# Kernel tuning notes

Hardware: AMD Instinct MI355X
Metric: run time of the kernel (lower is better)

Reference implementation:

```python
import jax, jax.numpy as jnp
import numpy as np

D_MODEL = 1024
NUM_HEADS = 16
HEAD_DIM = D_MODEL // NUM_HEADS
WINDOW = 256
NEG = -1000000000.0


def setup_inputs() -> dict:
    key = jax.random.key(0)
    ks = jax.random.split(key, 9)
    B, N, D = 2, 2048, D_MODEL
    s = 1.0 / np.sqrt(D)
    inp = {
        "x": jax.random.normal(ks[0], (B, N, D), dtype=jnp.float32),
        "Wq": jax.random.normal(ks[1], (D, D), dtype=jnp.float32) * s,
        "bq": jnp.zeros((D,), dtype=jnp.float32),
        "Wk": jax.random.normal(ks[2], (D, D), dtype=jnp.float32) * s,
        "bk": jnp.zeros((D,), dtype=jnp.float32),
        "Wv": jax.random.normal(ks[3], (D, D), dtype=jnp.float32) * s,
        "bv": jnp.zeros((D,), dtype=jnp.float32),
        "Wo": jax.random.normal(ks[4], (D, D), dtype=jnp.float32) * s,
        "bo": jnp.zeros((D,), dtype=jnp.float32),
    }
    return inp


def reference(x, Wq, bq, Wk, bk, Wv, bv, Wo, bo):
    B, N, D = x.shape
    H, hd = NUM_HEADS, HEAD_DIM
    q = (x @ Wq + bq).reshape(B, N, H, hd).transpose(0, 2, 1, 3)  # [B,H,N,hd]
    k = (x @ Wk + bk).reshape(B, N, H, hd).transpose(0, 2, 1, 3)
    v = (x @ Wv + bv).reshape(B, N, H, hd).transpose(0, 2, 1, 3)

    i = jnp.arange(N)[:, None]
    j = jnp.arange(N)[None, :]
    blocked = (j > i) | (j < i - WINDOW)  # causal + local window
    mask = jnp.where(blocked, jnp.float32(NEG), jnp.float32(0.0))  # [N,N]

    logits = jnp.einsum("bhid,bhjd->bhij", q, k) / jnp.sqrt(jnp.float32(hd))
    logits = logits + mask[None, None, :, :]
    attn = jax.nn.softmax(logits, axis=-1)
    out = jnp.einsum("bhij,bhjd->bhid", attn, v)  # [B,H,N,hd]
    out = out.transpose(0, 2, 1, 3).reshape(B, N, D)
    return out @ Wo + bo
```

## Files before the change

kernel.cpp:

```cpp
#include <hip/hip_runtime.h>


typedef unsigned short ushort_t;
typedef __bf16 bf16x8 __attribute__((ext_vector_type(8)));
typedef float f32x4 __attribute__((ext_vector_type(4)));
typedef unsigned short ushort8 __attribute__((ext_vector_type(8)));
typedef unsigned short ushort4v __attribute__((ext_vector_type(4)));

#define LOG2E 1.4426950408889634f

static __device__ __forceinline__ ushort_t f2b(float f) {
    union { float f; unsigned int u; } x;
    x.f = f;
    unsigned int u = x.u;
    unsigned int r = (u + 0x7FFFu + ((u >> 16) & 1u)) >> 16;
    return (ushort_t)r;
}

static __device__ __forceinline__ void store_out(float* p, float v) { *p = v; }
static __device__ __forceinline__ void store_out(ushort_t* p, float v) { *p = f2b(v); }

static __device__ __forceinline__ int sw(int row, int c) {
    return (row * 8 + (c ^ (row & 7))) * 8;
}

static __device__ __forceinline__ void gload_lds16(const ushort_t* g, ushort_t* l) {
    __builtin_amdgcn_global_load_lds(
        (const __attribute__((address_space(1))) void*)g,
        (__attribute__((address_space(3))) void*)l, 16, 0, 0);
}

__global__ __launch_bounds__(256) void prep_kernel(
    const float* __restrict__ x, ushort_t* __restrict__ xbf,
    const float* __restrict__ W0, const float* __restrict__ W1,
    const float* __restrict__ W2, const float* __restrict__ W3,
    ushort_t* __restrict__ T0, ushort_t* __restrict__ T1,
    ushort_t* __restrict__ T2, ushort_t* __restrict__ T3) {
    int tx = threadIdx.x, ty = threadIdx.y;
    if (blockIdx.z == 4) {
        int idx = (blockIdx.y * 32 + blockIdx.x) * 256 + ty * 32 + tx;
        int i = idx * 16;
#pragma unroll
        for (int half = 0; half < 2; half++) {
            f32x4 a = *(const f32x4*)&x[i + half * 8];
            f32x4 b = *(const f32x4*)&x[i + half * 8 + 4];
            ushort8 o;
#pragma unroll
            for (int e = 0; e < 4; e++) o[e] = f2b(a[e]);
#pragma unroll
            for (int e = 0; e < 4; e++) o[4 + e] = f2b(b[e]);
            *(ushort8*)&xbf[i + half * 8] = o;
        }
        return;
    }
    __shared__ ushort_t tile[32][33];
    const float* W;
    ushort_t* T;
    switch (blockIdx.z) {
        case 0: W = W0; T = T0; break;
        case 1: W = W1; T = T1; break;
        case 2: W = W2; T = T2; break;
        default: W = W3; T = T3; break;
    }
    int xx = blockIdx.x * 32 + tx;
    int ybase = blockIdx.y * 32 + ty;
#pragma unroll
    for (int r = 0; r < 4; r++) tile[ty + r * 8][tx] = f2b(W[(ybase + r * 8) * 1024 + xx]);
    __syncthreads();
    int xo = blockIdx.y * 32 + tx;
    int yobase = blockIdx.x * 32 + ty;
#pragma unroll
    for (int r = 0; r < 4; r++) T[(yobase + r * 8) * 1024 + xo] = tile[tx][ty + r * 8];
}

__global__ __launch_bounds__(256) void gemm_qkv_kernel(
    const ushort_t* __restrict__ A,
    const ushort_t* __restrict__ Bt0, const ushort_t* __restrict__ Bt1,
    const ushort_t* __restrict__ Bt2,
    const float* __restrict__ bias0, const float* __restrict__ bias1,
    const float* __restrict__ bias2,
    ushort_t* __restrict__ C0, ushort_t* __restrict__ C1, ushort_t* __restrict__ C2,
    float os0, float os1, float os2) {
    __shared__ ushort_t Al[64 * 64];
    __shared__ ushort_t Bl[128 * 64];

    const int id = blockIdx.x;
    const int xcd = id & 7;
    const int s = id >> 3;
    int m_blk = (xcd >> 1) * 16 + (s & 15);
    int ncol = (xcd & 1) * 12 + (s >> 4);
    int zsel = ncol >> 3;
    ncol &= 7;
    const int m0 = m_blk * 64;
    const int n0 = ncol * 128;

    const ushort_t* Bt;
    const float* bias;
    ushort_t* C;
    float oscale;
    if (zsel == 0) { Bt = Bt0; bias = bias0; C = C0; oscale = os0; }
    else if (zsel == 1) { Bt = Bt1; bias = bias1; C = C1; oscale = os1; }
    else { Bt = Bt2; bias = bias2; C = C2; oscale = os2; }

    const int tid = threadIdx.x;
    const int w = tid >> 6;
    const int l = tid & 63;
    const int wm = (w >> 1) * 32;
    const int wn = (w & 1) * 64;
    const int lrow = l & 15;
    const int lq = l >> 4;

    f32x4 acc[2][4];
#pragma unroll
    for (int mi = 0; mi < 2; mi++)
#pragma unroll
        for (int ni = 0; ni < 4; ni++) acc[mi][ni] = 0.0f;

    const int kt0 = (id * 5) & 15;
    for (int it = 0; it < 16; it++) {
        const int kt = ((kt0 + it) & 15) * 64;
#pragma unroll
        for (int t = 0; t < 2; t++) {
            int idx = t * 256 + tid;
            int row = idx >> 3, cs = idx & 7, c = cs ^ (row & 7);
            gload_lds16(&A[(long)(m0 + row) * 1024 + kt + c * 8], &Al[idx * 8]);
        }
#pragma unroll
        for (int t = 0; t < 4; t++) {
            int idx = t * 256 + tid;
            int row = idx >> 3, cs = idx & 7, c = cs ^ (row & 7);
            gload_lds16(&Bt[(long)(n0 + row) * 1024 + kt + c * 8], &Bl[idx * 8]);
        }
        __syncthreads();
#pragma unroll
        for (int ks = 0; ks < 64; ks += 32) {
            const int cb = (ks >> 3) + lq;
            bf16x8 af[2], bfr[4];
#pragma unroll
            for (int mi = 0; mi < 2; mi++)
                af[mi] = *(const bf16x8*)&Al[sw(wm + mi * 16 + lrow, cb)];
#pragma unroll
            for (int ni = 0; ni < 4; ni++)
                bfr[ni] = *(const bf16x8*)&Bl[sw(wn + ni * 16 + lrow, cb)];
#pragma unroll
            for (int mi = 0; mi < 2; mi++)
#pragma unroll
                for (int ni = 0; ni < 4; ni++)
                    acc[mi][ni] = __builtin_amdgcn_mfma_f32_16x16x32_bf16(
                        af[mi], bfr[ni], acc[mi][ni], 0, 0, 0);
        }
        __syncthreads();
    }

    if (zsel == 2) {
#pragma unroll
        for (int ni = 0; ni < 4; ni++) {
            int n = n0 + wn + ni * 16 + lrow;
            float bv = bias[n];
#pragma unroll
            for (int mi = 0; mi < 2; mi++) {
                int m = m0 + wm + mi * 16 + lq * 4;
                ushort4v o;
#pragma unroll
                for (int r = 0; r < 4; r++) o[r] = f2b((acc[mi][ni][r] + bv) * oscale);
                *(ushort4v*)&C[(long)n * 4096 + m] = o;
            }
        }
    } else {
#pragma unroll
        for (int ni = 0; ni < 4; ni++) {
            int n = n0 + wn + ni * 16 + lrow;
            float bv = bias[n];
#pragma unroll
            for (int mi = 0; mi < 2; mi++) {
#pragma unroll
                for (int r = 0; r < 4; r++) {
                    int m = m0 + wm + mi * 16 + lq * 4 + r;
                    store_out(&C[(long)m * 1024 + n], (acc[mi][ni][r] + bv) * oscale);
                }
            }
        }
    }
}

__global__ __launch_bounds__(256) void gemm_out_kernel(
    const ushort_t* __restrict__ A, const ushort_t* __restrict__ Bt,
    const float* __restrict__ bias, float* __restrict__ C) {
    __shared__ ushort_t Al[64 * 64];
    __shared__ ushort_t Bl[128 * 64];

    const int id = blockIdx.x;
    const int xcd = id & 7;
    const int s = id >> 3;
    const int m_blk = xcd * 8 + (s & 7);
    const int ncol = s >> 3;
    const int m0 = m_blk * 64;
    const int n0 = ncol * 128;

    const int tid = threadIdx.x;
    const int w = tid >> 6;
    const int l = tid & 63;
    const int wm = (w >> 1) * 32;
    const int wn = (w & 1) * 64;
    const int lrow = l & 15;
    const int lq = l >> 4;

    f32x4 acc[2][4];
#pragma unroll
    for (int mi = 0; mi < 2; mi++)
#pragma unroll
        for (int ni = 0; ni < 4; ni++) acc[mi][ni] = 0.0f;

    const int kt0 = (id * 5) & 15;
    for (int it = 0; it < 16; it++) {
        const int kt = ((kt0 + it) & 15) * 64;
#pragma unroll
        for (int t = 0; t < 2; t++) {
            int idx = t * 256 + tid;
            int row = idx >> 3, cs = idx & 7, c = cs ^ (row & 7);
            gload_lds16(&A[(long)(m0 + row) * 1024 + kt + c * 8], &Al[idx * 8]);
        }
#pragma unroll
        for (int t = 0; t < 4; t++) {
            int idx = t * 256 + tid;
            int row = idx >> 3, cs = idx & 7, c = cs ^ (row & 7);
            gload_lds16(&Bt[(long)(n0 + row) * 1024 + kt + c * 8], &Bl[idx * 8]);
        }
        __syncthreads();
#pragma unroll
        for (int ks = 0; ks < 64; ks += 32) {
            const int cb = (ks >> 3) + lq;
            bf16x8 af[2], bfr[4];
#pragma unroll
            for (int mi = 0; mi < 2; mi++)
                af[mi] = *(const bf16x8*)&Al[sw(wm + mi * 16 + lrow, cb)];
#pragma unroll
            for (int ni = 0; ni < 4; ni++)
                bfr[ni] = *(const bf16x8*)&Bl[sw(wn + ni * 16 + lrow, cb)];
#pragma unroll
            for (int mi = 0; mi < 2; mi++)
#pragma unroll
                for (int ni = 0; ni < 4; ni++)
                    acc[mi][ni] = __builtin_amdgcn_mfma_f32_16x16x32_bf16(
                        af[mi], bfr[ni], acc[mi][ni], 0, 0, 0);
        }
        __syncthreads();
    }

#pragma unroll
    for (int ni = 0; ni < 4; ni++) {
        int n = n0 + wn + ni * 16 + lrow;
        float bv = bias[n];
#pragma unroll
        for (int mi = 0; mi < 2; mi++) {
#pragma unroll
            for (int r = 0; r < 4; r++) {
                int m = m0 + wm + mi * 16 + lq * 4 + r;
                C[(long)m * 1024 + n] = acc[mi][ni][r] + bv;
            }
        }
    }
}

__global__ __launch_bounds__(256) void attn_kernel(
    const ushort_t* __restrict__ Q, const ushort_t* __restrict__ K,
    const ushort_t* __restrict__ VT, ushort_t* __restrict__ O) {
    __shared__ ushort_t Kl[128 * 64];
    __shared__ ushort_t Vtl[64 * 128];
    __shared__ ushort_t Pb[4 * 16 * 40];

    const int id = blockIdx.x;
    const int xcd = id & 7;
    const int s = id >> 3;
    const int bh = xcd * 4 + (s >> 5);
    const int b = bh >> 4;
    const int h = bh & 15;
    const int i0 = (s & 31) * 64;

    const int tid = threadIdx.x;
    const int w = tid >> 6;
    const int l = tid & 63;
    const int lrow = l & 15;
    const int lq = l >> 4;
    const int q0 = i0 + w * 16;

    const long baseBH = ((long)b * 2048) * 1024 + (long)h * 64;
    const long baseVT = (long)h * 64 * 4096 + (long)b * 2048;

    const ushort_t* qrow = Q + baseBH + (long)(q0 + lrow) * 1024;
    bf16x8 aq0 = *(const bf16x8*)&qrow[lq * 8];
    bf16x8 aq1 = *(const bf16x8*)&qrow[32 + lq * 8];

    float lpart[4];
    f32x4 oacc[4];
#pragma unroll
    for (int r = 0; r < 4; r++) lpart[r] = 0.0f;
#pragma unroll
    for (int ni = 0; ni < 4; ni++) oacc[ni] = 0.0f;

    const int kstart = (i0 - 256) > 0 ? (i0 - 256) : 0;
    const int kend = i0 + 64;
    ushort_t* Pw = &Pb[w * 16 * 40];

    for (int cs = kstart; cs < kend; cs += 128) {
        const int ce = (cs + 128 < kend) ? cs + 128 : kend;
#pragma unroll
        for (int t = 0; t < 4; t++) {
            int idx = t * 256 + tid;
            int rr = idx >> 3;
            int cc = idx & 7;
            int c = cc ^ (rr & 7);
            int key = cs + rr;
            key = key < 2047 ? key : 2047;
            gload_lds16(&K[baseBH + (long)key * 1024 + c * 8], &Kl[idx * 8]);
        }
#pragma unroll
        for (int t = 0; t < 4; t++) {
            int idx = t * 256 + tid;
            int rr = idx >> 4;
            int cc = idx & 15;
            int c = (cc & 8) | ((cc & 7) ^ (rr & 7));
            int kc = cs + c * 8;
            kc = kc < 2040 ? kc : 2040;
            gload_lds16(&VT[baseVT + (long)rr * 4096 + kc], &Vtl[idx * 8]);
        }
        __syncthreads();

        for (int kb = cs; kb < ce; kb += 32) {
            if (kb > q0 + 15 || kb + 31 < q0 - 256) continue;
            const int rb = kb - cs;
            f32x4 S0 = 0.0f, S1 = 0.0f;
            {
                bf16x8 bk;
                bk = *(const bf16x8*)&Kl[sw(rb + lrow, lq)];
                S0 = __builtin_amdgcn_mfma_f32_16x16x32_bf16(aq0, bk, S0, 0, 0, 0);
                bk = *(const bf16x8*)&Kl[sw(rb + lrow, 4 + lq)];
                S0 = __builtin_amdgcn_mfma_f32_16x16x32_bf16(aq1, bk, S0, 0, 0, 0);
                bk = *(const bf16x8*)&Kl[sw(rb + 16 + lrow, lq)];
                S1 = __builtin_amdgcn_mfma_f32_16x16x32_bf16(aq0, bk, S1, 0, 0, 0);
                bk = *(const bf16x8*)&Kl[sw(rb + 16 + lrow, 4 + lq)];
                S1 = __builtin_amdgcn_mfma_f32_16x16x32_bf16(aq1, bk, S1, 0, 0, 0);
            }
            const int col0 = kb + lrow;
            const int col1 = kb + 16 + lrow;
#pragma unroll
            for (int r = 0; r < 4; r++) {
                const int i = q0 + lq * 4 + r;
                float p0 = (col0 > i || col0 < i - 256) ? 0.0f : exp2f(S0[r] * LOG2E);
                float p1 = (col1 > i || col1 < i - 256) ? 0.0f : exp2f(S1[r] * LOG2E);
                lpart[r] += p0 + p1;
                const int prow = lq * 4 + r;
                Pw[prow * 40 + lrow] = f2b(p0);
                Pw[prow * 40 + 16 + lrow] = f2b(p1);
            }
            bf16x8 pf = *(const bf16x8*)&Pw[lrow * 40 + lq * 8];
#pragma unroll
            for (int ni = 0; ni < 4; ni++) {
                int ccg = (rb >> 3) + lq;
                int rsw = (ccg & 8) | ((ccg & 7) ^ (lrow & 7));
                bf16x8 vf = *(const bf16x8*)&Vtl[(ni * 16 + lrow) * 128 + rsw * 8];
                oacc[ni] = __builtin_amdgcn_mfma_f32_16x16x32_bf16(pf, vf, oacc[ni], 0, 0, 0);
            }
        }
        __syncthreads();
    }

    float lS[4];
#pragma unroll
    for (int r = 0; r < 4; r++) {
        float rs = lpart[r];
#pragma unroll
        for (int off = 8; off; off >>= 1) rs += __shfl_xor(rs, off, 64);
        lS[r] = rs;
    }

#pragma unroll
    for (int ni = 0; ni < 4; ni++) {
#pragma unroll
        for (int r = 0; r < 4; r++) {
            const int i = q0 + lq * 4 + r;
            const int d = ni * 16 + lrow;
            O[baseBH + (long)i * 1024 + d] = f2b(oacc[ni][r] / lS[r]);
        }
    }
}

extern "C" void kernel_launch(void* const* d_in, const int* in_sizes, int n_in,
                              void* d_out, int out_size, void* d_ws, size_t ws_size,
                              hipStream_t stream) {
    const float* x  = (const float*)d_in[0];
    const float* Wq = (const float*)d_in[1];
    const float* bq = (const float*)d_in[2];
    const float* Wk = (const float*)d_in[3];
    const float* bk = (const float*)d_in[4];
    const float* Wv = (const float*)d_in[5];
    const float* bv = (const float*)d_in[6];
    const float* Wo = (const float*)d_in[7];
    const float* bo = (const float*)d_in[8];
    float* out = (float*)d_out;

    ushort_t* ws = (ushort_t*)d_ws;
    const size_t WMAT = (size_t)1024 * 1024;
    const size_t ACT = (size_t)2 * 2048 * 1024;
    ushort_t* xbf = ws;
    ushort_t* Wqt = xbf + ACT;
    ushort_t* Wkt = Wqt + WMAT;
    ushort_t* Wvt = Wkt + WMAT;
    ushort_t* Wot = Wvt + WMAT;
    ushort_t* qws = Wot + WMAT;
    ushort_t* kws = qws + ACT;
    ushort_t* vws = kws + ACT;
    ushort_t* aws = xbf;

    prep_kernel<<<dim3(32, 32, 5), dim3(32, 8), 0, stream>>>(
        x, xbf, Wq, Wk, Wv, Wo, Wqt, Wkt, Wvt, Wot);

    gemm_qkv_kernel<<<1536, 256, 0, stream>>>(
        xbf, Wqt, Wkt, Wvt, bq, bk, bv, qws, kws, vws, 0.125f, 1.0f, 1.0f);

    attn_kernel<<<1024, 256, 0, stream>>>(qws, kws, vws, aws);

    gemm_out_kernel<<<512, 256, 0, stream>>>(aws, Wot, bo, out);
}
```

Baseline: 163.1 us.

## Double-buffer LDS tiles in QKV and output GEMMs to overlap loads with MFMA

Both GEMM kernels get two LDS buffers for the A and B tiles. The next k-tile is issued with global-to-LDS loads before computing on the current one, and a partial vmcnt wait plus raw s_barrier replaces the full __syncthreads. This is meant to hide global memory latency behind the MFMA work. It doubles LDS use to 48KB per block, which may reduce occupancy. The last iteration also prefetches a wrapped, redundant tile.

```diff
diff --git a/kernel.cpp b/kernel.cpp
--- a/kernel.cpp
+++ b/kernel.cpp
@@ -81,8 +81,8 @@
     const float* __restrict__ bias2,
     ushort_t* __restrict__ C0, ushort_t* __restrict__ C1, ushort_t* __restrict__ C2,
     float os0, float os1, float os2) {
-    __shared__ ushort_t Al[64 * 64];
-    __shared__ ushort_t Bl[128 * 64];
+    __shared__ ushort_t Al[2][64 * 64];
+    __shared__ ushort_t Bl[2][128 * 64];
 
     const int id = blockIdx.x;
     const int xcd = id & 7;
@@ -117,31 +117,43 @@
         for (int ni = 0; ni < 4; ni++) acc[mi][ni] = 0.0f;
 
     const int kt0 = (id * 5) & 15;
+
+    auto stage = [&](int bsel, int itv) {
+        const int kt = ((kt0 + itv) & 15) * 64;
+#pragma unroll
+        for (int t = 0; t < 2; t++) {
+            int idx = t * 256 + tid;
+            int row = idx >> 3, cc = idx & 7, c = cc ^ (row & 7);
+            gload_lds16(&A[(long)(m0 + row) * 1024 + kt + c * 8], &Al[bsel][idx * 8]);
+        }
+#pragma unroll
+        for (int t = 0; t < 4; t++) {
+            int idx = t * 256 + tid;
+            int row = idx >> 3, cc = idx & 7, c = cc ^ (row & 7);
+            gload_lds16(&Bt[(long)(n0 + row) * 1024 + kt + c * 8], &Bl[bsel][idx * 8]);
+        }
+    };
+
+    stage(0, 0);
+    int cur = 0;
     for (int it = 0; it < 16; it++) {
-        const int kt = ((kt0 + it) & 15) * 64;
-#pragma unroll
-        for (int t = 0; t < 2; t++) {
-            int idx = t * 256 + tid;
-            int row = idx >> 3, cs = idx & 7, c = cs ^ (row & 7);
-            gload_lds16(&A[(long)(m0 + row) * 1024 + kt + c * 8], &Al[idx * 8]);
-        }
-#pragma unroll
-        for (int t = 0; t < 4; t++) {
-            int idx = t * 256 + tid;
-            int row = idx >> 3, cs = idx & 7, c = cs ^ (row & 7);
-            gload_lds16(&Bt[(long)(n0 + row) * 1024 + kt + c * 8], &Bl[idx * 8]);
-        }
-        __syncthreads();
+        stage(cur ^ 1, it + 1);
+        asm volatile("s_waitcnt vmcnt(6)" ::: "memory");
+        __builtin_amdgcn_s_barrier();
+        asm volatile("" ::: "memory");
+        __builtin_amdgcn_sched_barrier(0);
+        const ushort_t* Ac = Al[cur];
+        const ushort_t* Bc = Bl[cur];
 #pragma unroll
         for (int ks = 0; ks < 64; ks += 32) {
             const int cb = (ks >> 3) + lq;
             bf16x8 af[2], bfr[4];
 #pragma unroll
             for (int mi = 0; mi < 2; mi++)
-                af[mi] = *(const bf16x8*)&Al[sw(wm + mi * 16 + lrow, cb)];
+                af[mi] = *(const bf16x8*)&Ac[sw(wm + mi * 16 + lrow, cb)];
 #pragma unroll
             for (int ni = 0; ni < 4; ni++)
-                bfr[ni] = *(const bf16x8*)&Bl[sw(wn + ni * 16 + lrow, cb)];
+                bfr[ni] = *(const bf16x8*)&Bc[sw(wn + ni * 16 + lrow, cb)];
 #pragma unroll
             for (int mi = 0; mi < 2; mi++)
 #pragma unroll
@@ -149,8 +161,12 @@
                     acc[mi][ni] = __builtin_amdgcn_mfma_f32_16x16x32_bf16(
                         af[mi], bfr[ni], acc[mi][ni], 0, 0, 0);
         }
-        __syncthreads();
-    }
+        __builtin_amdgcn_sched_barrier(0);
+        asm volatile("" ::: "memory");
+        __builtin_amdgcn_s_barrier();
+        cur ^= 1;
+    }
+    asm volatile("s_waitcnt vmcnt(0)" ::: "memory");
 
     if (zsel == 2) {
 #pragma unroll
@@ -186,8 +202,8 @@
 __global__ __launch_bounds__(256) void gemm_out_kernel(
     const ushort_t* __restrict__ A, const ushort_t* __restrict__ Bt,
     const float* __restrict__ bias, float* __restrict__ C) {
-    __shared__ ushort_t Al[64 * 64];
-    __shared__ ushort_t Bl[128 * 64];
+    __shared__ ushort_t Al[2][64 * 64];
+    __shared__ ushort_t Bl[2][128 * 64];
 
     const int id = blockIdx.x;
     const int xcd = id & 7;
@@ -212,31 +228,43 @@
         for (int ni = 0; ni < 4; ni++) acc[mi][ni] = 0.0f;
 
     const int kt0 = (id * 5) & 15;
+
+    auto stage = [&](int bsel, int itv) {
+        const int kt = ((kt0 + itv) & 15) * 64;
+#pragma unroll
+        for (int t = 0; t < 2; t++) {
+            int idx = t * 256 + tid;
+            int row = idx >> 3, cc = idx & 7, c = cc ^ (row & 7);
+            gload_lds16(&A[(long)(m0 + row) * 1024 + kt + c * 8], &Al[bsel][idx * 8]);
+        }
+#pragma unroll
+        for (int t = 0; t < 4; t++) {
+            int idx = t * 256 + tid;
+            int row = idx >> 3, cc = idx & 7, c = cc ^ (row & 7);
+            gload_lds16(&Bt[(long)(n0 + row) * 1024 + kt + c * 8], &Bl[bsel][idx * 8]);
+        }
+    };
+
+    stage(0, 0);
+    int cur = 0;
     for (int it = 0; it < 16; it++) {
-        const int kt = ((kt0 + it) & 15) * 64;
-#pragma unroll
-        for (int t = 0; t < 2; t++) {
-            int idx = t * 256 + tid;
-            int row = idx >> 3, cs = idx & 7, c = cs ^ (row & 7);
-            gload_lds16(&A[(long)(m0 + row) * 1024 + kt + c * 8], &Al[idx * 8]);
-        }
-#pragma unroll
-        for (int t = 0; t < 4; t++) {
-            int idx = t * 256 + tid;
-            int row = idx >> 3, cs = idx & 7, c = cs ^ (row & 7);
-            gload_lds16(&Bt[(long)(n0 + row) * 1024 + kt + c * 8], &Bl[idx * 8]);
-        }
-        __syncthreads();
+        stage(cur ^ 1, it + 1);
+        asm volatile("s_waitcnt vmcnt(6)" ::: "memory");
+        __builtin_amdgcn_s_barrier();
+        asm volatile("" ::: "memory");
+        __builtin_amdgcn_sched_barrier(0);
+        const ushort_t* Ac = Al[cur];
+        const ushort_t* Bc = Bl[cur];
 #pragma unroll
         for (int ks = 0; ks < 64; ks += 32) {
             const int cb = (ks >> 3) + lq;
             bf16x8 af[2], bfr[4];
 #pragma unroll
             for (int mi = 0; mi < 2; mi++)
-                af[mi] = *(const bf16x8*)&Al[sw(wm + mi * 16 + lrow, cb)];
+                af[mi] = *(const bf16x8*)&Ac[sw(wm + mi * 16 + lrow, cb)];
 #pragma unroll
             for (int ni = 0; ni < 4; ni++)
-                bfr[ni] = *(const bf16x8*)&Bl[sw(wn + ni * 16 + lrow, cb)];
+                bfr[ni] = *(const bf16x8*)&Bc[sw(wn + ni * 16 + lrow, cb)];
 #pragma unroll
             for (int mi = 0; mi < 2; mi++)
 #pragma unroll
@@ -244,8 +272,12 @@
                     acc[mi][ni] = __builtin_amdgcn_mfma_f32_16x16x32_bf16(
                         af[mi], bfr[ni], acc[mi][ni], 0, 0, 0);
         }
-        __syncthreads();
-    }
+        __builtin_amdgcn_sched_barrier(0);
+        asm volatile("" ::: "memory");
+        __builtin_amdgcn_s_barrier();
+        cur ^= 1;
+    }
+    asm volatile("s_waitcnt vmcnt(0)" ::: "memory");
 
 #pragma unroll
     for (int ni = 0; ni < 4; ni++) {
```

Measured after the change: 163.4 us. About the same (+0.2%).
